# Kernel tuning notes

Hardware: AMD Instinct MI355X
Metric: run time of the kernel (lower is better)

The kernel has to match this reference:

```python
import jax, jax.numpy as jnp
import numpy as np

# Config (from TheoreticalConfig, scaled to production size)
B = 4096          # batch_size
S = 128           # seq_len (max_seq_len)
DIM_Q = 512
DIM_Z = 64
DIM_U = 512
HID_V = 512       # assumed net_V hidden width
T_OFF = 20        # T_offline
T_ON = 10         # T_online
DT = 0.1
STIFF = 0.1       # stiffness
CSTIFF = 0.1      # contact_stiffness
MIN_DIM = min(DIM_U, DIM_Q)  # == DIM_Q here


def setup_inputs() -> dict:
    key = jax.random.key(0)
    ks = jax.random.split(key, 10)
    f32 = jnp.float32
    return {
        "u_seq": jax.random.normal(ks[0], (B, S, DIM_U), f32),
        "q0_off": jax.random.normal(ks[1], (B, DIM_Q), f32) * 0.1,
        "p0_off": jax.random.normal(ks[2], (B, DIM_Q), f32) * 0.1,
        "q0_on": jax.random.normal(ks[3], (B, DIM_Q), f32) * 0.1,
        "p0_on": jax.random.normal(ks[4], (B, DIM_Q), f32) * 0.1,
        "z": jax.random.normal(ks[5], (1, DIM_Z), f32) * 0.1,
        "W1": jax.random.normal(ks[6], (DIM_Q + DIM_Z, HID_V), f32) / np.sqrt(DIM_Q + DIM_Z).astype(np.float32),
        "b1": jnp.zeros((HID_V,), f32),
        "W2": jax.random.normal(ks[7], (HID_V, 1), f32) / np.sqrt(HID_V).astype(np.float32),
        "b2": jnp.zeros((1,), f32),
    }


def _net_V(qz, W1, b1, W2, b2):
    # small MLP potential: [B, dim_q+dim_z] -> [B, 1]
    return jnp.tanh(qz @ W1 + b1) @ W2 + b2


def _compute_H(q, p, s, z, W1, b1, W2, b2):
    # H^c = K + V_quad + V_net + Phi, all [B, 1]
    K = 0.5 * jnp.sum(p * p, axis=-1, keepdims=True)
    V_quad = 0.5 * STIFF * jnp.sum(q * q, axis=-1, keepdims=True)
    V_net = _net_V(jnp.concatenate([q, z], axis=-1), W1, b1, W2, b2)
    Phi = 0.5 * CSTIFF * s * s
    return K + V_quad + V_net + Phi


def reference(u_seq, q0_off, p0_off, q0_on, p0_on, z, W1, b1, W2, b2):
    zb = jnp.broadcast_to(z, (B, DIM_Z))
    s = jnp.zeros((B, 1), u_seq.dtype)

    # ---- evolve_offline: symplectic-ish leapfrog with friction, T_OFF-1 steps ----
    F0_off = _compute_H(q0_off, p0_off, s, zb, W1, b1, W2, b2)

    def off_step(carry, _):
        q, p = carry
        q_new = q + DT * p                     # q += dt * grad_p (grad_p = p)
        p_new = (p - DT * (STIFF * q)) * 0.99  # p -= dt * grad_q (grad_q = stiff*q_old), then damping
        return (q_new, p_new), None

    (qf, pf), _ = jax.lax.scan(off_step, (q0_off, p0_off), None, length=T_OFF - 1)
    Ff_off = _compute_H(qf, pf, s, zb, W1, b1, W2, b2)
    offline_F = jnp.concatenate([F0_off, Ff_off], axis=1)  # [B, 2]

    # ---- evolve_online: port-coupled integration for min(S, T_ON) steps ----
    F0_on = _compute_H(q0_on, p0_on, s, zb, W1, b1, W2, b2)
    steps = min(S, T_ON)

    def on_step(carry, u_t):
        q, p = carry
        # p_new[:, :MIN_DIM] = p - dt*stiff*q + dt*0.1*u_t ; MIN_DIM == DIM_Q so full update
        p_new = (p - DT * (STIFF * q) + DT * (0.1 * u_t)) * 0.99
        q_new = q + DT * p_new
        return (q_new, p_new), None

    u_scan = jnp.transpose(u_seq[:, :steps, :MIN_DIM], (1, 0, 2))  # [steps, B, dim_q]
    (qf2, pf2), _ = jax.lax.scan(on_step, (q0_on, p0_on), u_scan)
    Ff_on = _compute_H(qf2, pf2, s, zb, W1, b1, W2, b2)
    online_F = jnp.concatenate([F0_on, Ff_on], axis=1)  # [B, 2]

    q_trajectory = qf2[:, None, :]  # [B, 1, dim_q]
    return offline_F, online_F, q_trajectory
```

## Files before the change

kernel.cpp:

```cpp
#include <hip/hip_runtime.h>
#include <hip/hip_bf16.h>

#define BB 4096
#define SS 128
#define DIMQ 512
#define DIMZ 64
#define HIDV 512

typedef __attribute__((ext_vector_type(8))) short sh8;
typedef __attribute__((ext_vector_type(4))) float f32x4;
typedef __attribute__((ext_vector_type(4))) unsigned short us4;

__device__ inline unsigned short f2bf(float f) {
    unsigned u = __float_as_uint(f);
    return (unsigned short)((u + 0x7fffu + ((u >> 16) & 1u)) >> 16);
}

__global__ __launch_bounds__(256) void k_states_prep(
        const float* __restrict__ u, const float* __restrict__ q0off,
        const float* __restrict__ p0off, const float* __restrict__ q0on,
        const float* __restrict__ p0on, const float* __restrict__ b2,
        const float* __restrict__ W1, const float* __restrict__ z,
        const float* __restrict__ b1,
        unsigned short* __restrict__ Qall, unsigned short* __restrict__ W1qT,
        float* __restrict__ cvec, float* __restrict__ out,
        float* __restrict__ qtraj,
        float R00, float R01, float R10, float R11) {
    if (blockIdx.x >= 2048) {
        int pbi = blockIdx.x - 2048;
        __shared__ float tile[32][33];
        int bx = pbi & 15, by = pbi >> 4;
        int k0 = by * 32, n0 = bx * 32;
        int tx = threadIdx.x & 31, tg = threadIdx.x >> 5;
        #pragma unroll
        for (int rr = 0; rr < 4; rr++) {
            int ty = tg * 4 + rr;
            tile[ty][tx] = W1[(size_t)(k0 + ty) * HIDV + n0 + tx];
        }
        __syncthreads();
        #pragma unroll
        for (int rr = 0; rr < 4; rr++) {
            int ty = tg * 4 + rr;
            W1qT[(size_t)(n0 + ty) * DIMQ + k0 + tx] = f2bf(tile[tx][ty]);
        }
        if (pbi < 2) {
            int h = pbi * 256 + threadIdx.x;
            float acc = b1[h];
            #pragma unroll 8
            for (int k = 0; k < DIMZ; k++) acc += z[k] * W1[(size_t)(DIMQ + k) * HIDV + h];
            cvec[h] = acc;
        }
        return;
    }
    int t = threadIdx.x;
    int half = t >> 7;
    int tc = t & 127;
    int b = blockIdx.x * 2 + half;
    int j = tc * 4;
    size_t idx = (size_t)b * DIMQ + j;
    float q[4], p[4], qo[4], po[4];
    *(float4*)q  = *(const float4*)(q0off + idx);
    *(float4*)p  = *(const float4*)(p0off + idx);
    *(float4*)qo = *(const float4*)(q0on + idx);
    *(float4*)po = *(const float4*)(p0on + idx);

    float sums[8] = {0, 0, 0, 0, 0, 0, 0, 0};
    us4 w0, w1, w2, w3;
    float q2[4], p2[4];
    #pragma unroll
    for (int c = 0; c < 4; c++) {
        float qq = q[c], pp = p[c];
        sums[0] += qq * qq;
        sums[1] += pp * pp;
        float qf = R00 * qq + R01 * pp;
        float pf = R10 * qq + R11 * pp;
        sums[2] += qf * qf;
        sums[3] += pf * pf;
        w0[c] = f2bf(qq);
        w1[c] = f2bf(qf);
        q2[c] = qo[c]; p2[c] = po[c];
        sums[4] += q2[c] * q2[c];
        sums[5] += p2[c] * p2[c];
        w2[c] = f2bf(q2[c]);
    }
    *(us4*)(Qall + idx) = w0;
    *(us4*)(Qall + (size_t)(BB + b) * DIMQ + j) = w1;
    *(us4*)(Qall + (size_t)(2 * BB + b) * DIMQ + j) = w2;

    const float* ub = u + (size_t)b * SS * DIMQ + j;
    #pragma unroll
    for (int st = 0; st < 10; st++) {
        float uv[4];
        *(float4*)uv = *(const float4*)(ub + (size_t)st * DIMQ);
        #pragma unroll
        for (int c = 0; c < 4; c++) {
            p2[c] = (p2[c] - 0.1f * (0.1f * q2[c]) + 0.1f * (0.1f * uv[c])) * 0.99f;
            q2[c] = q2[c] + 0.1f * p2[c];
        }
    }
    #pragma unroll
    for (int c = 0; c < 4; c++) {
        sums[6] += q2[c] * q2[c];
        sums[7] += p2[c] * p2[c];
        w3[c] = f2bf(q2[c]);
    }
    *(us4*)(Qall + (size_t)(3 * BB + b) * DIMQ + j) = w3;
    *(float4*)(qtraj + idx) = *(float4*)q2;

    __shared__ float red[2][2][8];
    int lane = t & 63, wv = (t >> 6) & 1;
    #pragma unroll
    for (int k = 0; k < 8; k++) {
        float v = sums[k];
        #pragma unroll
        for (int m = 1; m < 64; m <<= 1) v += __shfl_xor(v, m, 64);
        if (lane == 0) red[half][wv][k] = v;
    }
    __syncthreads();
    if (tc < 4) {
        int e = tc;
        float sq = red[half][0][2 * e] + red[half][1][2 * e];
        float sp = red[half][0][2 * e + 1] + red[half][1][2 * e + 1];
        float F = 0.5f * sp + 0.05f * sq + b2[0];
        size_t o = (size_t)b * 2 + (e & 1) + (size_t)(e >> 1) * 2 * BB;
        out[o] = F;
    }
}

__global__ __launch_bounds__(256) void k_gemm(
        const unsigned short* __restrict__ Qall, const unsigned short* __restrict__ W1qT,
        const float* __restrict__ cvec, const float* __restrict__ W2,
        float* __restrict__ out) {
    __shared__ __attribute__((aligned(16))) char lds[65536];
    const int t = threadIdx.x;
    const int lane = t & 63;
    const int w = t >> 6;
    const int wr = w >> 1, wc = w & 1;
    const int rowBase = blockIdx.x * 128;
    const int colBase = blockIdx.y * 128;

    f32x4 acc[4][4] = {};

    auto STAGE = [&](int kt, int buf) {
        char* ldsA = lds + buf * 32768;
        char* ldsB = ldsA + 16384;
        #pragma unroll
        for (int i = 0; i < 4; i++) {
            unsigned chunk = i * 256 + t;
            unsigned r = chunk >> 3;
            unsigned scb = (chunk & 7) ^ (r & 7);
            const unsigned short* srcA = Qall + (size_t)(rowBase + r) * 512 + (unsigned)kt * 64 + scb * 8;
            __builtin_amdgcn_global_load_lds(
                (const __attribute__((address_space(1))) unsigned int*)(const void*)srcA,
                (__attribute__((address_space(3))) unsigned int*)(void*)(ldsA + chunk * 16), 16, 0, 0);
            const unsigned short* srcB = W1qT + (size_t)(colBase + r) * 512 + (unsigned)kt * 64 + scb * 8;
            __builtin_amdgcn_global_load_lds(
                (const __attribute__((address_space(1))) unsigned int*)(const void*)srcB,
                (__attribute__((address_space(3))) unsigned int*)(void*)(ldsB + chunk * 16), 16, 0, 0);
        }
    };

    STAGE(0, 0);
    asm volatile("s_waitcnt vmcnt(0)" ::: "memory");
    __builtin_amdgcn_s_barrier();

    for (int kt = 0; kt < 8; kt++) {
        int cur = kt & 1;
        if (kt < 7) STAGE(kt + 1, cur ^ 1);
        char* ldsA = lds + cur * 32768;
        char* ldsB = ldsA + 16384;
        #pragma unroll
        for (int ks = 0; ks < 2; ks++) {
            sh8 af[4], bf_[4];
            int kb = ks * 64 + ((lane >> 4) << 4);
            #pragma unroll
            for (int mi = 0; mi < 4; mi++) {
                int m = wr * 64 + mi * 16 + (lane & 15);
                af[mi] = *(const sh8*)(ldsA + m * 128 + (kb ^ ((m & 7) << 4)));
            }
            #pragma unroll
            for (int ni = 0; ni < 4; ni++) {
                int n = wc * 64 + ni * 16 + (lane & 15);
                bf_[ni] = *(const sh8*)(ldsB + n * 128 + (kb ^ ((n & 7) << 4)));
            }
            #pragma unroll
            for (int mi = 0; mi < 4; mi++)
                #pragma unroll
                for (int ni = 0; ni < 4; ni++)
                    acc[mi][ni] = __builtin_amdgcn_mfma_f32_16x16x32_bf16(af[mi], bf_[ni], acc[mi][ni], 0, 0, 0);
        }
        asm volatile("s_waitcnt vmcnt(0) lgkmcnt(0)" ::: "memory");
        __builtin_amdgcn_s_barrier();
    }

    float w2v[4], cv[4];
    #pragma unroll
    for (int ni = 0; ni < 4; ni++) {
        int n = colBase + wc * 64 + ni * 16 + (lane & 15);
        w2v[ni] = W2[n];
        cv[ni] = cvec[n];
    }
    #pragma unroll
    for (int mi = 0; mi < 4; mi++) {
        #pragma unroll
        for (int r = 0; r < 4; r++) {
            float partial = 0.f;
            #pragma unroll
            for (int ni = 0; ni < 4; ni++)
                partial += tanhf(acc[mi][ni][r] + cv[ni]) * w2v[ni];
            partial += __shfl_xor(partial, 1, 64);
            partial += __shfl_xor(partial, 2, 64);
            partial += __shfl_xor(partial, 4, 64);
            partial += __shfl_xor(partial, 8, 64);
            if ((lane & 15) == 0) {
                int row = rowBase + wr * 64 + mi * 16 + ((lane >> 4) << 2) + r;
                int e = row >> 12, bb = row & 4095;
                size_t o = (size_t)bb * 2 + (e & 1) + (size_t)(e >> 1) * 2 * BB;
                atomicAdd(out + o, partial);
            }
        }
    }
}

extern "C" void kernel_launch(void* const* d_in, const int* in_sizes, int n_in,
                              void* d_out, int out_size, void* d_ws, size_t ws_size,
                              hipStream_t stream) {
    const float* u     = (const float*)d_in[0];
    const float* q0off = (const float*)d_in[1];
    const float* p0off = (const float*)d_in[2];
    const float* q0on  = (const float*)d_in[3];
    const float* p0on  = (const float*)d_in[4];
    const float* z     = (const float*)d_in[5];
    const float* W1    = (const float*)d_in[6];
    const float* b1    = (const float*)d_in[7];
    const float* W2    = (const float*)d_in[8];
    const float* b2    = (const float*)d_in[9];
    float* out = (float*)d_out;

    char* ws = (char*)d_ws;
    unsigned short* Qall = (unsigned short*)ws;
    unsigned short* W1qT = (unsigned short*)(ws + 16777216);
    float* cvec = (float*)(ws + 16777216 + 524288);

    double a00 = 1, a01 = 0, a10 = 0, a11 = 1;
    const double m00 = 1.0, m01 = 0.1, m10 = -0.1 * 0.1 * 0.99, m11 = 0.99;
    for (int i = 0; i < 19; i++) {
        double n00 = m00 * a00 + m01 * a10;
        double n01 = m00 * a01 + m01 * a11;
        double n10 = m10 * a00 + m11 * a10;
        double n11 = m10 * a01 + m11 * a11;
        a00 = n00; a01 = n01; a10 = n10; a11 = n11;
    }

    k_states_prep<<<2304, 256, 0, stream>>>(u, q0off, p0off, q0on, p0on, b2,
                                            W1, z, b1, Qall, W1qT, cvec, out,
                                            out + 4 * BB,
                                            (float)a00, (float)a01, (float)a10, (float)a11);
    k_gemm<<<dim3(128, 4), 256, 0, stream>>>(Qall, W1qT, cvec, W2, out);
}
```

Baseline: 43.26 us.

## Fuse bf16 state conversion into GEMM A-loads and use fast tanh

Stops writing the bf16 Qall staging buffer in the prep kernel. The GEMM now loads the fp32 states directly (q0off, q0off/p0off combined via the propagator for the final offline state, q0on, qtraj), converts them to bf16 in registers and writes them swizzled into LDS. This removes the 16 MB bf16 write and read round trip. The cost is that fp32 A-tiles are read once per column tile, four times in total, and the offline final state needs two arrays. The epilogue's tanhf is also replaced with an exp plus reciprocal approximation.

```diff
diff --git a/kernel.cpp b/kernel.cpp
--- a/kernel.cpp
+++ b/kernel.cpp
@@ -9,11 +9,15 @@
 
 typedef __attribute__((ext_vector_type(8))) short sh8;
 typedef __attribute__((ext_vector_type(4))) float f32x4;
-typedef __attribute__((ext_vector_type(4))) unsigned short us4;
 
 __device__ inline unsigned short f2bf(float f) {
     unsigned u = __float_as_uint(f);
     return (unsigned short)((u + 0x7fffu + ((u >> 16) & 1u)) >> 16);
+}
+
+__device__ __forceinline__ float fast_tanh(float x) {
+    float e = __expf(2.0f * x);
+    return 1.0f - 2.0f * __builtin_amdgcn_rcpf(e + 1.0f);
 }
 
 __global__ __launch_bounds__(256) void k_states_prep(
@@ -22,9 +26,8 @@
         const float* __restrict__ p0on, const float* __restrict__ b2,
         const float* __restrict__ W1, const float* __restrict__ z,
         const float* __restrict__ b1,
-        unsigned short* __restrict__ Qall, unsigned short* __restrict__ W1qT,
-        float* __restrict__ cvec, float* __restrict__ out,
-        float* __restrict__ qtraj,
+        unsigned short* __restrict__ W1qT, float* __restrict__ cvec,
+        float* __restrict__ out, float* __restrict__ qtraj,
         float R00, float R01, float R10, float R11) {
     if (blockIdx.x >= 2048) {
         int pbi = blockIdx.x - 2048;
@@ -65,7 +68,6 @@
     *(float4*)po = *(const float4*)(p0on + idx);
 
     float sums[8] = {0, 0, 0, 0, 0, 0, 0, 0};
-    us4 w0, w1, w2, w3;
     float q2[4], p2[4];
     #pragma unroll
     for (int c = 0; c < 4; c++) {
@@ -76,17 +78,10 @@
         float pf = R10 * qq + R11 * pp;
         sums[2] += qf * qf;
         sums[3] += pf * pf;
-        w0[c] = f2bf(qq);
-        w1[c] = f2bf(qf);
         q2[c] = qo[c]; p2[c] = po[c];
         sums[4] += q2[c] * q2[c];
         sums[5] += p2[c] * p2[c];
-        w2[c] = f2bf(q2[c]);
-    }
-    *(us4*)(Qall + idx) = w0;
-    *(us4*)(Qall + (size_t)(BB + b) * DIMQ + j) = w1;
-    *(us4*)(Qall + (size_t)(2 * BB + b) * DIMQ + j) = w2;
-
+    }
     const float* ub = u + (size_t)b * SS * DIMQ + j;
     #pragma unroll
     for (int st = 0; st < 10; st++) {
@@ -102,9 +97,7 @@
     for (int c = 0; c < 4; c++) {
         sums[6] += q2[c] * q2[c];
         sums[7] += p2[c] * p2[c];
-        w3[c] = f2bf(q2[c]);
-    }
-    *(us4*)(Qall + (size_t)(3 * BB + b) * DIMQ + j) = w3;
+    }
     *(float4*)(qtraj + idx) = *(float4*)q2;
 
     __shared__ float red[2][2][8];
@@ -128,47 +121,83 @@
 }
 
 __global__ __launch_bounds__(256) void k_gemm(
-        const unsigned short* __restrict__ Qall, const unsigned short* __restrict__ W1qT,
-        const float* __restrict__ cvec, const float* __restrict__ W2,
-        float* __restrict__ out) {
+        const float* __restrict__ q0off, const float* __restrict__ p0off,
+        const float* __restrict__ q0on, const float* __restrict__ qtraj,
+        const unsigned short* __restrict__ W1qT, const float* __restrict__ cvec,
+        const float* __restrict__ W2, float* __restrict__ out,
+        float R00, float R01) {
     __shared__ __attribute__((aligned(16))) char lds[65536];
     const int t = threadIdx.x;
     const int lane = t & 63;
     const int w = t >> 6;
     const int wr = w >> 1, wc = w & 1;
-    const int rowBase = blockIdx.x * 128;
-    const int colBase = blockIdx.y * 128;
+    const int rt = blockIdx.x >> 2;
+    const int colBase = (blockIdx.x & 3) * 128;
+    const int e = rt >> 5;
+    const int batchBase = (rt & 31) * 128;
+    const bool isE1 = (e == 1);
+    const float* srcA = (e == 0) ? q0off : (e == 1) ? q0off : (e == 2) ? q0on : qtraj;
 
     f32x4 acc[4][4] = {};
-
-    auto STAGE = [&](int kt, int buf) {
-        char* ldsA = lds + buf * 32768;
-        char* ldsB = ldsA + 16384;
+    float4 Aq[4][2], Ap[4][2];
+
+    auto LOAD_A = [&](int kt) {
         #pragma unroll
         for (int i = 0; i < 4; i++) {
-            unsigned chunk = i * 256 + t;
-            unsigned r = chunk >> 3;
-            unsigned scb = (chunk & 7) ^ (r & 7);
-            const unsigned short* srcA = Qall + (size_t)(rowBase + r) * 512 + (unsigned)kt * 64 + scb * 8;
+            int ch = i * 256 + t, r = ch >> 3, cb = ch & 7;
+            const float* ba = srcA + (size_t)(batchBase + r) * 512 + kt * 64 + cb * 8;
+            Aq[i][0] = *(const float4*)ba;
+            Aq[i][1] = *(const float4*)(ba + 4);
+            if (isE1) {
+                const float* bp = p0off + (size_t)(batchBase + r) * 512 + kt * 64 + cb * 8;
+                Ap[i][0] = *(const float4*)bp;
+                Ap[i][1] = *(const float4*)(bp + 4);
+            }
+        }
+    };
+    auto WRITE_A = [&](int buf) {
+        char* dA = lds + buf * 16384;
+        #pragma unroll
+        for (int i = 0; i < 4; i++) {
+            int ch = i * 256 + t, r = ch >> 3, cb = ch & 7;
+            sh8 v;
+            #pragma unroll
+            for (int c2 = 0; c2 < 8; c2++) {
+                float qv = (c2 < 4) ? Aq[i][0][c2] : Aq[i][1][c2 - 4];
+                if (isE1) {
+                    float pv = (c2 < 4) ? Ap[i][0][c2] : Ap[i][1][c2 - 4];
+                    qv = R00 * qv + R01 * pv;
+                }
+                v[c2] = (short)f2bf(qv);
+            }
+            *(sh8*)(dA + r * 128 + ((cb << 4) ^ ((r & 7) << 4))) = v;
+        }
+    };
+    auto STAGE_B = [&](int kt, int buf) {
+        char* dB = lds + 32768 + buf * 16384;
+        #pragma unroll
+        for (int i = 0; i < 4; i++) {
+            unsigned ch = i * 256 + t;
+            unsigned r = ch >> 3;
+            unsigned scb = (ch & 7) ^ (r & 7);
+            const unsigned short* src = W1qT + (size_t)(colBase + r) * 512 + (unsigned)kt * 64 + scb * 8;
             __builtin_amdgcn_global_load_lds(
-                (const __attribute__((address_space(1))) unsigned int*)(const void*)srcA,
-                (__attribute__((address_space(3))) unsigned int*)(void*)(ldsA + chunk * 16), 16, 0, 0);
-            const unsigned short* srcB = W1qT + (size_t)(colBase + r) * 512 + (unsigned)kt * 64 + scb * 8;
-            __builtin_amdgcn_global_load_lds(
-                (const __attribute__((address_space(1))) unsigned int*)(const void*)srcB,
-                (__attribute__((address_space(3))) unsigned int*)(void*)(ldsB + chunk * 16), 16, 0, 0);
+                (const __attribute__((address_space(1))) unsigned int*)(const void*)src,
+                (__attribute__((address_space(3))) unsigned int*)(void*)(dB + ch * 16), 16, 0, 0);
         }
     };
 
-    STAGE(0, 0);
-    asm volatile("s_waitcnt vmcnt(0)" ::: "memory");
+    LOAD_A(0);
+    STAGE_B(0, 0);
+    WRITE_A(0);
+    asm volatile("s_waitcnt vmcnt(0) lgkmcnt(0)" ::: "memory");
     __builtin_amdgcn_s_barrier();
 
     for (int kt = 0; kt < 8; kt++) {
         int cur = kt & 1;
-        if (kt < 7) STAGE(kt + 1, cur ^ 1);
-        char* ldsA = lds + cur * 32768;
-        char* ldsB = ldsA + 16384;
+        if (kt < 7) { LOAD_A(kt + 1); STAGE_B(kt + 1, cur ^ 1); }
+        char* ldsA = lds + cur * 16384;
+        char* ldsB = lds + 32768 + cur * 16384;
         #pragma unroll
         for (int ks = 0; ks < 2; ks++) {
             sh8 af[4], bf_[4];
@@ -189,6 +218,7 @@
                 for (int ni = 0; ni < 4; ni++)
                     acc[mi][ni] = __builtin_amdgcn_mfma_f32_16x16x32_bf16(af[mi], bf_[ni], acc[mi][ni], 0, 0, 0);
         }
+        if (kt < 7) WRITE_A(cur ^ 1);
         asm volatile("s_waitcnt vmcnt(0) lgkmcnt(0)" ::: "memory");
         __builtin_amdgcn_s_barrier();
     }
@@ -207,15 +237,14 @@
             float partial = 0.f;
             #pragma unroll
             for (int ni = 0; ni < 4; ni++)
-                partial += tanhf(acc[mi][ni][r] + cv[ni]) * w2v[ni];
+                partial += fast_tanh(acc[mi][ni][r] + cv[ni]) * w2v[ni];
             partial += __shfl_xor(partial, 1, 64);
             partial += __shfl_xor(partial, 2, 64);
             partial += __shfl_xor(partial, 4, 64);
             partial += __shfl_xor(partial, 8, 64);
             if ((lane & 15) == 0) {
-                int row = rowBase + wr * 64 + mi * 16 + ((lane >> 4) << 2) + r;
-                int e = row >> 12, bb = row & 4095;
-                size_t o = (size_t)bb * 2 + (e & 1) + (size_t)(e >> 1) * 2 * BB;
+                int b = batchBase + wr * 64 + mi * 16 + ((lane >> 4) << 2) + r;
+                size_t o = (size_t)b * 2 + (e & 1) + (size_t)(e >> 1) * 2 * BB;
                 atomicAdd(out + o, partial);
             }
         }
@@ -236,11 +265,11 @@
     const float* W2    = (const float*)d_in[8];
     const float* b2    = (const float*)d_in[9];
     float* out = (float*)d_out;
+    float* qtraj = out + 4 * BB;
 
     char* ws = (char*)d_ws;
-    unsigned short* Qall = (unsigned short*)ws;
-    unsigned short* W1qT = (unsigned short*)(ws + 16777216);
-    float* cvec = (float*)(ws + 16777216 + 524288);
+    unsigned short* W1qT = (unsigned short*)ws;
+    float* cvec = (float*)(ws + 524288);
 
     double a00 = 1, a01 = 0, a10 = 0, a11 = 1;
     const double m00 = 1.0, m01 = 0.1, m10 = -0.1 * 0.1 * 0.99, m11 = 0.99;
@@ -253,8 +282,9 @@
     }
 
     k_states_prep<<<2304, 256, 0, stream>>>(u, q0off, p0off, q0on, p0on, b2,
-                                            W1, z, b1, Qall, W1qT, cvec, out,
-                                            out + 4 * BB,
+                                            W1, z, b1, W1qT, cvec, out,
+                                            qtraj,
                                             (float)a00, (float)a01, (float)a10, (float)a11);
-    k_gemm<<<dim3(128, 4), 256, 0, stream>>>(Qall, W1qT, cvec, W2, out);
-}
+    k_gemm<<<512, 256, 0, stream>>>(q0off, p0off, q0on, qtraj, W1qT, cvec, W2,
+                                    out, (float)a00, (float)a01);
+}
```

Measured after the change: 53.13 us. 22.8% more time.
